# Performance work log

Hardware: AMD Instinct MI355X
Metric: run time of the kernel (lower is better)

The kernel has to match this reference:

```python
import jax, jax.numpy as jnp
import numpy as np

N_E = 1_600_000
D = 128
N_OUT = 100_000


def setup_inputs() -> dict:
    key = jax.random.key(0)
    k1, k2, k3, k4 = jax.random.split(key, 4)
    e = jax.random.normal(k1, (N_E, D), dtype=jnp.float32)
    index = jax.random.randint(k2, (N_E,), 0, N_OUT, dtype=jnp.int64)
    # Linear params (torch nn.Linear: y = x @ W.T + b), kaiming-ish scale
    W = jax.random.normal(k3, (D, D), dtype=jnp.float32) / np.sqrt(D)
    b = jax.random.normal(k4, (D,), dtype=jnp.float32) * 0.01
    return {"e": e, "index": index, "W": W, "b": b}


def reference(e, index, W, b):
    # Linear + ReLU: (n_e, d)
    h = jax.nn.relu(jnp.einsum("nd,kd->nk", e, W) + b)
    # Scatter-sum along dim 0 into n_outputs rows
    out = jax.ops.segment_sum(h, index, num_segments=N_OUT)
    return out
```

## Files before the change

### kernel.cpp

```cpp
#include <hip/hip_runtime.h>
#include <hip/hip_bf16.h>

#define DIM 128
#define N_SEG 100000
#define N_TOT (N_SEG + 1)
#define NB 98

typedef __attribute__((ext_vector_type(8))) __bf16 bf16x8;
typedef __attribute__((ext_vector_type(4))) float f32x4;

#define WS_OFF 64
#define WS_RUN (WS_OFF + N_TOT + 1)
#define WS_BSUM (WS_RUN + N_SEG)
#define WS_BPRE (WS_BSUM + 128)
#define WS_UNITS (WS_BPRE + 128)
#define WS_ORDER (WS_UNITS + 600000)

__global__ void idx_probe_kernel(const unsigned* __restrict__ idx32,
                                 unsigned* __restrict__ flag, int n) {
  unsigned v = 0;
  const int stride = gridDim.x * blockDim.x;
  for (int i = blockIdx.x * blockDim.x + threadIdx.x; i < n; i += stride)
    v |= idx32[2 * i + 1];
  if (v) atomicOr(flag, 1u);
}

__global__ void hist_kernel(const uint4* __restrict__ idx4,
                            const unsigned* __restrict__ flag,
                            unsigned* __restrict__ cnt, int n) {
  const bool idx64 = (*flag == 0u);
  const int stride = gridDim.x * blockDim.x;
  const int t0 = blockIdx.x * blockDim.x + threadIdx.x;
  if (idx64) {
    const int nv = n >> 1;
    for (int i = t0; i < nv; i += stride) {
      const uint4 v = idx4[i];
      atomicAdd(&cnt[v.x], 1u);
      atomicAdd(&cnt[v.z], 1u);
    }
  } else {
    const int nv = n >> 2;
    for (int i = t0; i < nv; i += stride) {
      const uint4 v = idx4[i];
      atomicAdd(&cnt[v.x], 1u);
      atomicAdd(&cnt[v.y], 1u);
      atomicAdd(&cnt[v.z], 1u);
      atomicAdd(&cnt[v.w], 1u);
    }
  }
}

__global__ __launch_bounds__(1024) void scan_bsum(const unsigned* __restrict__ off,
                                                  unsigned* __restrict__ bsum) {
  __shared__ unsigned ws[16];
  const int t = threadIdx.x;
  const int i = blockIdx.x * 1024 + t;
  unsigned v = (i < N_TOT) ? off[i] : 0u;
#pragma unroll
  for (int d = 1; d < 64; d <<= 1) v += __shfl_xor(v, d);
  if ((t & 63) == 0) ws[t >> 6] = v;
  __syncthreads();
  if (t == 0) {
    unsigned s = 0;
#pragma unroll
    for (int w = 0; w < 16; ++w) s += ws[w];
    bsum[blockIdx.x] = s;
  }
}

__global__ __launch_bounds__(128) void scan_btop(unsigned* __restrict__ bsum,
                                                 unsigned* __restrict__ bpre) {
  __shared__ unsigned part[128];
  const int t = threadIdx.x;
  unsigned v = (t < NB) ? bsum[t] : 0u;
  part[t] = v;
  __syncthreads();
  for (int d = 1; d < 128; d <<= 1) {
    const unsigned u = (t >= d) ? part[t - d] : 0u;
    __syncthreads();
    part[t] += u;
    __syncthreads();
  }
  bpre[t] = part[t] - v;
}

__global__ __launch_bounds__(1024) void scan_fixup(unsigned* __restrict__ off,
                                                   unsigned* __restrict__ run,
                                                   const unsigned* __restrict__ bpre) {
  __shared__ unsigned wsum[16], wpre[16];
  const int t = threadIdx.x;
  const int lane = t & 63;
  const int wv = t >> 6;
  const int i = blockIdx.x * 1024 + t;
  const unsigned v = (i < N_TOT) ? off[i] : 0u;
  unsigned s = v;
#pragma unroll
  for (int d = 1; d < 64; d <<= 1) {
    const unsigned u = __shfl_up(s, d);
    if (lane >= d) s += u;
  }
  if (lane == 63) wsum[wv] = s;
  __syncthreads();
  if (t < 16) {
    unsigned w = wsum[t];
    unsigned ps = w;
#pragma unroll
    for (int d = 1; d < 16; d <<= 1) {
      const unsigned u = __shfl_up(ps, d, 16);
      if (t >= d) ps += u;
    }
    wpre[t] = ps - w;
  }
  __syncthreads();
  const unsigned excl = (s - v) + wpre[wv] + bpre[blockIdx.x];
  if (i < N_TOT) off[i] = excl;
  if (i < N_SEG) run[i] = excl;
}

__global__ void rank_kernel(const uint4* __restrict__ idx4,
                            const unsigned* __restrict__ flag,
                            unsigned* __restrict__ run,
                            unsigned* __restrict__ order, int n) {
  const bool idx64 = (*flag == 0u);
  const int stride = gridDim.x * blockDim.x;
  const int t0 = blockIdx.x * blockDim.x + threadIdx.x;
  if (idx64) {
    const int nv = n >> 1;
    for (int i = t0; i < nv; i += stride) {
      const uint4 v = idx4[i];
      unsigned p0 = atomicAdd(&run[v.x], 1u);
      order[p0] = 2u * i;
      unsigned p1 = atomicAdd(&run[v.z], 1u);
      order[p1] = 2u * i + 1u;
    }
  } else {
    const int nv = n >> 2;
    for (int i = t0; i < nv; i += stride) {
      const uint4 v = idx4[i];
      unsigned p0 = atomicAdd(&run[v.x], 1u);
      order[p0] = 4u * i;
      unsigned p1 = atomicAdd(&run[v.y], 1u);
      order[p1] = 4u * i + 1u;
      unsigned p2 = atomicAdd(&run[v.z], 1u);
      order[p2] = 4u * i + 2u;
      unsigned p3 = atomicAdd(&run[v.w], 1u);
      order[p3] = 4u * i + 3u;
    }
  }
}

__global__ void unit_build(const unsigned* __restrict__ off,
                           uint2* __restrict__ units,
                           unsigned* __restrict__ ucnt) {
  const int s = blockIdx.x * blockDim.x + threadIdx.x;
  if (s >= N_SEG) return;
  const unsigned b = off[s];
  const unsigned c = off[s + 1] - b;
  if (c == 0) return;
  const unsigned nu = (c + 15) >> 4;
  const unsigned pos = atomicAdd(ucnt, nu);
  const unsigned solo = (nu == 1) ? (1u << 23) : 0u;
  for (unsigned t = 0; t < nu; ++t) {
    const unsigned cnt = min(16u, c - 16u * t);
    uint2 ent;
    ent.x = b + 16u * t;
    ent.y = (unsigned)s | ((cnt - 1u) << 17) | solo;
    units[pos + t] = ent;
  }
}

__global__ __launch_bounds__(256, 2) void fused_main(
    const float* __restrict__ e, const float* __restrict__ W,
    const float* __restrict__ bias_p, const unsigned* __restrict__ order,
    const uint2* __restrict__ units, const unsigned* __restrict__ ucnt,
    float* __restrict__ out) {
  __shared__ bf16x8 wlds[2048];

  const int tid = threadIdx.x;
  const int wave = tid >> 6;
  const int lane = tid & 63;
  const int lr = lane & 15;
  const int lg = lane >> 4;

#pragma unroll
  for (int j = 0; j < 8; ++j) {
    const int g = (tid << 3) | j;
    const int gl = g & 63;
    const int tt = (g >> 6) & 3;
    const int k0 = g >> 8;
    const int row = k0 * 16 + (gl & 15);
    const int col = tt * 32 + (gl >> 4) * 8;
    const float* src = W + (size_t)row * DIM + col;
    f32x4 w0 = *(const f32x4*)src;
    f32x4 w1 = *(const f32x4*)(src + 4);
    bf16x8 f;
    f[0] = (__bf16)w0[0]; f[1] = (__bf16)w0[1];
    f[2] = (__bf16)w0[2]; f[3] = (__bf16)w0[3];
    f[4] = (__bf16)w1[0]; f[5] = (__bf16)w1[1];
    f[6] = (__bf16)w1[2]; f[7] = (__bf16)w1[3];
    wlds[g] = f;
  }
  __syncthreads();

  float bias[8];
#pragma unroll
  for (int k0 = 0; k0 < 8; ++k0) bias[k0] = bias_p[k0 * 16 + lr];

  const int n_units = (int)*ucnt;
  const int wid = blockIdx.x * 4 + wave;
  const int nw = gridDim.x * 4;
  if (wid >= n_units) return;

  uint2 eA = units[wid];
  uint2 eB = units[(wid + nw < n_units) ? wid + nw : n_units - 1];
  uint2 eC = units[(wid + 2 * nw < n_units) ? wid + 2 * nw : n_units - 1];

  {
    const int cA = (int)((eA.y >> 17) & 15u) + 1;
    const unsigned idA = order[eA.x + (lr < cA ? lr : cA - 1)];
    (void)idA;
  }
  const int cA0 = (int)((eA.y >> 17) & 15u) + 1;
  unsigned idCur = order[eA.x + (lr < cA0 ? lr : cA0 - 1)];
  f32x4 eload[8];
  {
    const float* erow = e + (size_t)idCur * DIM + lg * 8;
#pragma unroll
    for (int t = 0; t < 4; ++t) {
      eload[2 * t]     = *(const f32x4*)(erow + t * 32);
      eload[2 * t + 1] = *(const f32x4*)(erow + t * 32 + 4);
    }
  }
  const int cB0 = (int)((eB.y >> 17) & 15u) + 1;
  unsigned idNext = order[eB.x + (lr < cB0 ? lr : cB0 - 1)];

  for (int u = wid; u < n_units; u += nw) {
    const int seg = (int)(eA.y & 0x1FFFFu);
    const int cnt = (int)((eA.y >> 17) & 15u) + 1;
    const bool solo = (eA.y >> 23) & 1u;

    bf16x8 afrag[4];
#pragma unroll
    for (int t = 0; t < 4; ++t) {
      f32x4 a0 = eload[2 * t], a1 = eload[2 * t + 1];
      bf16x8 f;
      f[0] = (__bf16)a0[0]; f[1] = (__bf16)a0[1];
      f[2] = (__bf16)a0[2]; f[3] = (__bf16)a0[3];
      f[4] = (__bf16)a1[0]; f[5] = (__bf16)a1[1];
      f[6] = (__bf16)a1[2]; f[7] = (__bf16)a1[3];
      afrag[t] = f;
    }

    {
      const float* erow = e + (size_t)idNext * DIM + lg * 8;
#pragma unroll
      for (int t = 0; t < 4; ++t) {
        eload[2 * t]     = *(const f32x4*)(erow + t * 32);
        eload[2 * t + 1] = *(const f32x4*)(erow + t * 32 + 4);
      }
    }
    {
      const int cC = (int)((eC.y >> 17) & 15u) + 1;
      idNext = order[eC.x + (lr < cC ? lr : cC - 1)];
    }
    uint2 eC_next =
        units[(u + 3 * nw < n_units) ? u + 3 * nw : n_units - 1];

    float colsum[8] = {0.f, 0.f, 0.f, 0.f, 0.f, 0.f, 0.f, 0.f};
#pragma unroll
    for (int half = 0; half < 2; ++half) {
      f32x4 acc[4];
#pragma unroll
      for (int k = 0; k < 4; ++k) acc[k] = (f32x4){0.f, 0.f, 0.f, 0.f};
#pragma unroll
      for (int t = 0; t < 4; ++t) {
#pragma unroll
        for (int k = 0; k < 4; ++k) {
          bf16x8 bf = wlds[((half * 4 + k) * 4 + t) * 64 + lane];
          acc[k] = __builtin_amdgcn_mfma_f32_16x16x32_bf16(afrag[t], bf,
                                                           acc[k], 0, 0, 0);
        }
      }
#pragma unroll
      for (int r = 0; r < 4; ++r) {
        const bool valid = (lg * 4 + r) < cnt;
#pragma unroll
        for (int k = 0; k < 4; ++k) {
          const float v = fmaxf(acc[k][r] + bias[half * 4 + k], 0.f);
          colsum[half * 4 + k] += valid ? v : 0.f;
        }
      }
    }

#pragma unroll
    for (int k0 = 0; k0 < 8; ++k0) {
      float s = colsum[k0];
      s += __shfl_xor(s, 16);
      s += __shfl_xor(s, 32);
      colsum[k0] = s;
    }
    if (lg == 0) {
      float* orow = out + (size_t)seg * DIM + lr;
      if (solo) {
#pragma unroll
        for (int k0 = 0; k0 < 8; ++k0) orow[k0 * 16] = colsum[k0];
      } else {
#pragma unroll
        for (int k0 = 0; k0 < 8; ++k0)
          unsafeAtomicAdd(orow + k0 * 16, colsum[k0]);
      }
    }

    eA = eB;
    eB = eC;
    eC = eC_next;
  }
}

extern "C" void kernel_launch(void* const* d_in, const int* in_sizes, int n_in,
                              void* d_out, int out_size, void* d_ws, size_t ws_size,
                              hipStream_t stream) {
  const float* e = (const float*)d_in[0];
  const int* idx = (const int*)d_in[1];
  const float* W = (const float*)d_in[2];
  const float* b = (const float*)d_in[3];
  float* out = (float*)d_out;
  unsigned* ws32 = (unsigned*)d_ws;

  const int n_e = in_sizes[0] / DIM;

  hipMemsetAsync(d_ws, 0, (size_t)WS_RUN * sizeof(unsigned), stream);
  hipMemsetAsync(d_out, 0, (size_t)out_size * sizeof(float), stream);

  idx_probe_kernel<<<64, 256, 0, stream>>>((const unsigned*)idx, ws32,
                                           n_e / 2);
  hist_kernel<<<1024, 256, 0, stream>>>((const uint4*)idx, ws32, ws32 + WS_OFF,
                                        n_e);
  scan_bsum<<<NB, 1024, 0, stream>>>(ws32 + WS_OFF, ws32 + WS_BSUM);
  scan_btop<<<1, 128, 0, stream>>>(ws32 + WS_BSUM, ws32 + WS_BPRE);
  scan_fixup<<<NB, 1024, 0, stream>>>(ws32 + WS_OFF, ws32 + WS_RUN,
                                      ws32 + WS_BPRE);
  rank_kernel<<<1024, 256, 0, stream>>>((const uint4*)idx, ws32, ws32 + WS_RUN,
                                        ws32 + WS_ORDER, n_e);
  unit_build<<<(N_SEG + 255) / 256, 256, 0, stream>>>(
      ws32 + WS_OFF, (uint2*)(ws32 + WS_UNITS), ws32 + 1);
  fused_main<<<2048, 256, 0, stream>>>(e, W, b, ws32 + WS_ORDER,
                                       (const uint2*)(ws32 + WS_UNITS),
                                       ws32 + 1, out);
}
```

Before: 459.1 us.

## Fuse unit building and selective output zeroing into scan fixup kernel

Unit construction moves into the scan fixup kernel, which uses a wave-level prefix sum so there is one atomic per wave instead of one per segment. The full memset of the output is replaced by zeroing only rows that are empty or span several units, since solo segments are presumably written directly by the main kernel. The memset of the run array is dropped because scan_fixup overwrites it anyway, a dead prefetch load in fused_main is removed, and the probe kernel grid is enlarged. This saves a launch and most of the output memset traffic, but correctness now depends on solo rows being fully stored rather than accumulated.

```diff
diff --git a/kernel.cpp b/kernel.cpp
--- a/kernel.cpp
+++ b/kernel.cpp
@@ -84,9 +84,10 @@
   bpre[t] = part[t] - v;
 }
 
-__global__ __launch_bounds__(1024) void scan_fixup(unsigned* __restrict__ off,
-                                                   unsigned* __restrict__ run,
-                                                   const unsigned* __restrict__ bpre) {
+__global__ __launch_bounds__(1024) void scan_fixup_build(
+    unsigned* __restrict__ off, unsigned* __restrict__ run,
+    const unsigned* __restrict__ bpre, uint2* __restrict__ units,
+    unsigned* __restrict__ ucnt, float* __restrict__ out) {
   __shared__ unsigned wsum[16], wpre[16];
   const int t = threadIdx.x;
   const int lane = t & 63;
@@ -115,6 +116,32 @@
   const unsigned excl = (s - v) + wpre[wv] + bpre[blockIdx.x];
   if (i < N_TOT) off[i] = excl;
   if (i < N_SEG) run[i] = excl;
+
+  const unsigned c = (i < N_SEG) ? v : 0u;
+  const unsigned nu = (c + 15u) >> 4;
+  if (i < N_SEG && (c == 0u || nu > 1u)) {
+    f32x4* orow = (f32x4*)(out + (size_t)i * DIM);
+#pragma unroll
+    for (int k = 0; k < DIM / 4; ++k) orow[k] = (f32x4){0.f, 0.f, 0.f, 0.f};
+  }
+  unsigned inc = nu;
+#pragma unroll
+  for (int d = 1; d < 64; d <<= 1) {
+    const unsigned u = __shfl_up(inc, d);
+    if (lane >= d) inc += u;
+  }
+  unsigned base = 0;
+  if (lane == 63 && inc > 0) base = atomicAdd(ucnt, inc);
+  base = __shfl(base, 63);
+  unsigned pos = base + inc - nu;
+  const unsigned solo = (nu == 1u) ? (1u << 23) : 0u;
+  for (unsigned k = 0; k < nu; ++k) {
+    const unsigned cnt = min(16u, c - 16u * k);
+    uint2 ent;
+    ent.x = excl + 16u * k;
+    ent.y = (unsigned)i | ((cnt - 1u) << 17) | solo;
+    units[pos + k] = ent;
+  }
 }
 
 __global__ void rank_kernel(const uint4* __restrict__ idx4,
@@ -146,26 +173,6 @@
       unsigned p3 = atomicAdd(&run[v.w], 1u);
       order[p3] = 4u * i + 3u;
     }
-  }
-}
-
-__global__ void unit_build(const unsigned* __restrict__ off,
-                           uint2* __restrict__ units,
-                           unsigned* __restrict__ ucnt) {
-  const int s = blockIdx.x * blockDim.x + threadIdx.x;
-  if (s >= N_SEG) return;
-  const unsigned b = off[s];
-  const unsigned c = off[s + 1] - b;
-  if (c == 0) return;
-  const unsigned nu = (c + 15) >> 4;
-  const unsigned pos = atomicAdd(ucnt, nu);
-  const unsigned solo = (nu == 1) ? (1u << 23) : 0u;
-  for (unsigned t = 0; t < nu; ++t) {
-    const unsigned cnt = min(16u, c - 16u * t);
-    uint2 ent;
-    ent.x = b + 16u * t;
-    ent.y = (unsigned)s | ((cnt - 1u) << 17) | solo;
-    units[pos + t] = ent;
   }
 }
 
@@ -215,11 +222,6 @@
   uint2 eB = units[(wid + nw < n_units) ? wid + nw : n_units - 1];
   uint2 eC = units[(wid + 2 * nw < n_units) ? wid + 2 * nw : n_units - 1];
 
-  {
-    const int cA = (int)((eA.y >> 17) & 15u) + 1;
-    const unsigned idA = order[eA.x + (lr < cA ? lr : cA - 1)];
-    (void)idA;
-  }
   const int cA0 = (int)((eA.y >> 17) & 15u) + 1;
   unsigned idCur = order[eA.x + (lr < cA0 ? lr : cA0 - 1)];
   f32x4 eload[8];
@@ -329,21 +331,19 @@
 
   const int n_e = in_sizes[0] / DIM;
 
-  hipMemsetAsync(d_ws, 0, (size_t)WS_RUN * sizeof(unsigned), stream);
-  hipMemsetAsync(d_out, 0, (size_t)out_size * sizeof(float), stream);
-
-  idx_probe_kernel<<<64, 256, 0, stream>>>((const unsigned*)idx, ws32,
-                                           n_e / 2);
+  hipMemsetAsync(d_ws, 0, (size_t)(WS_OFF + N_TOT) * sizeof(unsigned), stream);
+
+  idx_probe_kernel<<<304, 256, 0, stream>>>((const unsigned*)idx, ws32,
+                                            n_e / 2);
   hist_kernel<<<1024, 256, 0, stream>>>((const uint4*)idx, ws32, ws32 + WS_OFF,
                                         n_e);
   scan_bsum<<<NB, 1024, 0, stream>>>(ws32 + WS_OFF, ws32 + WS_BSUM);
   scan_btop<<<1, 128, 0, stream>>>(ws32 + WS_BSUM, ws32 + WS_BPRE);
-  scan_fixup<<<NB, 1024, 0, stream>>>(ws32 + WS_OFF, ws32 + WS_RUN,
-                                      ws32 + WS_BPRE);
+  scan_fixup_build<<<NB, 1024, 0, stream>>>(
+      ws32 + WS_OFF, ws32 + WS_RUN, ws32 + WS_BPRE,
+      (uint2*)(ws32 + WS_UNITS), ws32 + 1, out);
   rank_kernel<<<1024, 256, 0, stream>>>((const uint4*)idx, ws32, ws32 + WS_RUN,
                                         ws32 + WS_ORDER, n_e);
-  unit_build<<<(N_SEG + 255) / 256, 256, 0, stream>>>(
-      ws32 + WS_OFF, (uint2*)(ws32 + WS_UNITS), ws32 + 1);
   fused_main<<<2048, 256, 0, stream>>>(e, W, b, ws32 + WS_ORDER,
                                        (const uint2*)(ws32 + WS_UNITS),
                                        ws32 + 1, out);
```

After: 451.8 us. About the same (-1.6%).
